# Optimization experiments

Hardware: AMD Instinct MI355X
Metric: run time of the kernel (lower is better)

## Reference

```python
import jax, jax.numpy as jnp
import numpy as np

N, E = 100000, 3200000
D_IN, D_H, H, C, TDIM, N_CLS = 17, 32, 2, 16, 32, 2


def _seg_softmax(alpha, dst, num_segments):
    # numerically stable softmax over edges grouped by destination node
    m = jax.ops.segment_max(alpha, dst, num_segments=num_segments)  # [N,H]
    a = jnp.exp(alpha - m[dst])
    s = jax.ops.segment_sum(a, dst, num_segments=num_segments)      # [N,H]
    return a / s[dst]


def setup_inputs() -> dict:
    key = jax.random.key(0)
    ks = jax.random.split(key, 16)
    w = lambda k, o, i: jax.random.normal(k, (o, i), dtype=jnp.float32) * 0.05
    inp = {
        "x": jax.random.normal(ks[0], (N, D_IN), dtype=jnp.float32),
        "edge_index": jax.random.randint(ks[1], (2, E), 0, N, dtype=jnp.int64),
        "t": jax.random.uniform(ks[2], (E, 1), dtype=jnp.float32),
        "node_time": jax.random.uniform(ks[3], (N,), dtype=jnp.float32),
        # TimeEncode params (init exactly as torch module)
        "basis_freq": jnp.asarray(1.0 / 10 ** np.linspace(0, 9, TDIM), dtype=jnp.float32),
        "phase": jnp.zeros((TDIM,), dtype=jnp.float32),
        # lin: 17 -> 32
        "W_lin": w(ks[4], D_H, D_IN), "b_lin": jnp.zeros((D_H,), jnp.float32),
        # TransformerConv(32, 16, heads=2, edge_dim=32)
        "Wq": w(ks[5], H * C, D_H), "bq": jnp.zeros((H * C,), jnp.float32),
        "Wk": w(ks[6], H * C, D_H), "bk": jnp.zeros((H * C,), jnp.float32),
        "Wv": w(ks[7], H * C, D_H), "bv": jnp.zeros((H * C,), jnp.float32),
        "We": w(ks[8], H * C, TDIM), "be": jnp.zeros((H * C,), jnp.float32),
        "Wskip": w(ks[9], H * C, D_H), "bskip": jnp.zeros((H * C,), jnp.float32),
        # out: 32 -> 2
        "W_out": w(ks[10], N_CLS, D_H), "b_out": jnp.zeros((N_CLS,), jnp.float32),
    }
    return inp


def reference(x, edge_index, t, node_time, basis_freq, phase, W_lin, b_lin,
              Wq, bq, Wk, bk, Wv, bv, We, be, Wskip, bskip, W_out, b_out):
    src, dst = edge_index[0], edge_index[1]
    n = x.shape[0]
    # relative time per edge + cosine time encoding -> [E, 32]
    rel_t = node_time[src][:, None] - t                      # [E,1]
    rel_t_enc = jnp.cos(rel_t * basis_freq[None, :] + phase[None, :])  # [E,32]
    # node MLP
    h1 = jax.nn.relu(x @ W_lin.T + b_lin)                    # [N,32]
    # TransformerConv (dropout off / eval mode)
    q = (h1 @ Wq.T + bq)[dst].reshape(-1, H, C)              # [E,H,C]
    e = (rel_t_enc @ We.T + be).reshape(-1, H, C)            # [E,H,C]
    k = (h1 @ Wk.T + bk)[src].reshape(-1, H, C) + e
    alpha = (q * k).sum(-1) / jnp.sqrt(jnp.float32(C))       # [E,H]
    alpha = _seg_softmax(alpha, dst, n)
    v = (h1 @ Wv.T + bv)[src].reshape(-1, H, C) + e          # [E,H,C]
    msg = (v * alpha[:, :, None]).reshape(-1, H * C)         # [E,32]
    agg = jax.ops.segment_sum(msg, dst, num_segments=n)      # [N,32]
    h = agg + h1 @ Wskip.T + bskip                           # root/skip connection
    logits = h @ W_out.T + b_out                             # [N,2]
    return jax.nn.log_softmax(logits, axis=1)
```

## Files before the change

kernel.cpp:

```cpp
#include <hip/hip_runtime.h>
#include <math.h>

#define D_IN 17
#define DH   32
#define TDIM 32
#define TABK 128

#define NBSH 8
#define BNODES (1 << NBSH)
#define NBKMAX 512
#define CAPB 9216
#define TILE 8192

#define SM_BYTES 53248

typedef float v2f __attribute__((ext_vector_type(2)));

__global__ __launch_bounds__(64) void build_table(
    const float* __restrict__ We, const float* __restrict__ be,
    const float* __restrict__ freq, const float* __restrict__ phase,
    float* __restrict__ table, int* __restrict__ bcur)
{
    if (blockIdx.x == 0) {
        for (int i = threadIdx.x; i < NBKMAX; i += 64) bcur[i] = 0;
    }
    int k = blockIdx.x * blockDim.x + threadIdx.x;
    if (k > TABK) return;
    float r = -1.0f + 2.0f * (float)k / (float)TABK;
    float cj[TDIM];
#pragma unroll
    for (int j = 0; j < TDIM; ++j) cj[j] = cosf(r * freq[j] + phase[j]);
#pragma unroll 4
    for (int o = 0; o < DH; ++o) {
        float acc = be[o];
#pragma unroll
        for (int j = 0; j < TDIM; ++j) acc += cj[j] * We[o * TDIM + j];
        table[(size_t)k * DH + o] = acc;
    }
}

__global__ __launch_bounds__(512) void fused_np_s1(
    const float* __restrict__ x,
    const float* __restrict__ Wl, const float* __restrict__ bl,
    const float* __restrict__ Wq, const float* __restrict__ bq,
    const float* __restrict__ Wk, const float* __restrict__ bk,
    const float* __restrict__ Wv, const float* __restrict__ bv,
    const float* __restrict__ Ws, const float* __restrict__ bs,
    float* __restrict__ qn, unsigned char* __restrict__ kvn,
    float* __restrict__ skv, int N,
    const int* __restrict__ ei, const float* __restrict__ t,
    const float* __restrict__ ntime,
    int* __restrict__ bcur, int* __restrict__ stgA,
    int E, int NBK, int NA, int NB)
{
    __shared__ __align__(16) char smraw[SM_BYTES];

    int bid = blockIdx.x;
    int tid = threadIdx.x;

    int grp = bid / 3, rem = bid - grp * 3;
    bool isA;
    int ridx;
    if (grp < NB) {
        if (rem < 2) { isA = true;  ridx = grp * 2 + rem; }
        else         { isA = false; ridx = grp; }
    } else {
        isA = true;  ridx = 2 * NB + (bid - 3 * NB);
    }

    if (isA) {
        if (ridx >= NA) return;
        float* w = (float*)smraw;
        int mat  = ridx & 3;
        int xblk = ridx >> 2;

        {
            const float* Wsel = (mat == 0) ? Wq : (mat == 1) ? Wk : (mat == 2) ? Wv : Ws;
            const float* bsel = (mat == 0) ? bq : (mat == 1) ? bk : (mat == 2) ? bv : bs;
            for (int idx = tid; idx < 544; idx += 512) {
                int i = idx / D_IN, j = idx - i * D_IN;
                w[j * DH + i] = Wl[idx];
            }
            if (tid < 32) w[544 + tid] = bl[tid];
            for (int i = tid; i < 1024; i += 512) w[576 + i] = Wsel[i];
            if (tid < 32) w[1600 + tid] = bsel[tid];
        }
        __syncthreads();

        int n = xblk * 512 + tid;
        if (n >= N) return;

        float xv[D_IN];
#pragma unroll
        for (int j = 0; j < D_IN; ++j) xv[j] = x[(size_t)n * D_IN + j];

        float h1[DH];
#pragma unroll
        for (int c = 0; c < 8; ++c) {
            float4 b = *(const float4*)&w[544 + c * 4];
            h1[c*4+0] = b.x; h1[c*4+1] = b.y; h1[c*4+2] = b.z; h1[c*4+3] = b.w;
        }
#pragma unroll
        for (int j = 0; j < D_IN; ++j) {
            float xj = xv[j];
#pragma unroll
            for (int c = 0; c < 8; ++c) {
                float4 wv = *(const float4*)&w[j * DH + c * 4];
                h1[c*4+0] += xj * wv.x;
                h1[c*4+1] += xj * wv.y;
                h1[c*4+2] += xj * wv.z;
                h1[c*4+3] += xj * wv.w;
            }
        }
#pragma unroll
        for (int i = 0; i < DH; ++i) h1[i] = fmaxf(h1[i], 0.0f);

        float outr[DH];
#pragma unroll
        for (int i = 0; i < DH; ++i) {
            float acc = w[1600 + i];
#pragma unroll
            for (int c = 0; c < 8; ++c) {
                float4 wv = *(const float4*)&w[576 + i * DH + c * 4];
                acc += h1[c * 4 + 0] * wv.x + h1[c * 4 + 1] * wv.y
                     + h1[c * 4 + 2] * wv.z + h1[c * 4 + 3] * wv.w;
            }
            outr[i] = acc;
        }

        if (mat == 0) {
            float4* dst4 = (float4*)(qn + (size_t)n * DH);
#pragma unroll
            for (int c = 0; c < 8; ++c) {
                float4 o; o.x = outr[c*4+0] * 0.25f; o.y = outr[c*4+1] * 0.25f;
                o.z = outr[c*4+2] * 0.25f; o.w = outr[c*4+3] * 0.25f;
                dst4[c] = o;
            }
        } else if (mat == 1 || mat == 2) {
            unsigned int pw[8];
#pragma unroll
            for (int i = 0; i < 8; ++i) {
                int pk = 0;
                pk = __builtin_amdgcn_cvt_pk_fp8_f32(outr[4*i+0], outr[4*i+1], pk, false);
                pk = __builtin_amdgcn_cvt_pk_fp8_f32(outr[4*i+2], outr[4*i+3], pk, true);
                pw[i] = (unsigned int)pk;
            }
            uint4* row = (uint4*)(kvn + (size_t)n * 64) + (mat == 1 ? 0 : 2);
            uint4 o0; o0.x = pw[0]; o0.y = pw[1]; o0.z = pw[2]; o0.w = pw[3];
            uint4 o1; o1.x = pw[4]; o1.y = pw[5]; o1.z = pw[6]; o1.w = pw[7];
            row[0] = o0;
            row[1] = o1;
        } else {
            float4* dst4 = (float4*)(skv + (size_t)n * DH);
#pragma unroll
            for (int c = 0; c < 8; ++c) {
                float4 o; o.x = outr[c*4+0]; o.y = outr[c*4+1];
                o.z = outr[c*4+2]; o.w = outr[c*4+3];
                dst4[c] = o;
            }
        }
        return;
    }

    int*            tileW = (int*)smraw;
    unsigned short* tileB = (unsigned short*)(smraw + 32768);
    int*            sd    = (int*)(smraw + 32768);
    int*            lcnt  = (int*)(smraw + 49152);
    int*            lcur  = (int*)(smraw + 51200);
    int*            gdel  = lcnt;

    int base = ridx * TILE;
    int cnt_here = min(TILE, E - base);

    lcnt[tid] = 0;
    __syncthreads();

    int dreg[TILE / 512];
#pragma unroll
    for (int i = 0; i < TILE / 512; ++i) {
        int e = base + i * 512 + tid;
        if (e < E) {
            int d = ei[E + e];
            dreg[i] = d;
            atomicAdd(&lcnt[((unsigned int)d) >> NBSH], 1);
        } else {
            dreg[i] = -1;
        }
    }
    __syncthreads();

    {
        int v0 = lcnt[tid];
        int lane = tid & 63, wv = tid >> 6;
        int val = v0;
#pragma unroll
        for (int st = 1; st < 64; st <<= 1) {
            int nb = __shfl_up(val, st);
            if (lane >= st) val += nb;
        }
        if (lane == 63) sd[wv] = val;
        __syncthreads();
        int woff = 0;
#pragma unroll
        for (int k2 = 0; k2 < 7; ++k2) woff += (k2 < wv) ? sd[k2] : 0;
        int lofs = woff + val - v0;
        if (tid < NBK) {
            int gpos = (v0 > 0) ? (tid * CAPB + atomicAdd(&bcur[tid], v0)) : 0;
            lcur[tid] = lofs;
            gdel[tid] = gpos - lofs;
        }
    }
    __syncthreads();

#pragma unroll 4
    for (int i = 0; i < TILE / 512; ++i) {
        int d = dreg[i];
        if (d >= 0) {
            int e = base + i * 512 + tid;
            int s = ei[e];
            float rel = ntime[s] - t[e];
            float u = fmaf(rel, (float)(TABK / 2), (float)(TABK / 2) + 0.5f);
            int idx = (int)u;
            idx = min(max(idx, 0), TABK - 1);
            int b = ((unsigned int)d) >> NBSH;
            int r = atomicAdd(&lcur[b], 1);
            tileW[r] = s | (idx << 17) | ((d & (BNODES - 1)) << 24);
            tileB[r] = (unsigned short)b;
        }
    }
    __syncthreads();

    for (int k = tid; k < cnt_here; k += 512) {
        int b = (int)tileB[k];
        int gp = gdel[b] + k;
        if (gp >= b * CAPB && gp < (b + 1) * CAPB) {
            stgA[gp] = tileW[k];
        }
    }
}

__global__ __launch_bounds__(1024) void s2_hist_scatter(
    const int* __restrict__ bcur, const int* __restrict__ stgA,
    int* __restrict__ payload, int* __restrict__ off, int* __restrict__ cntout,
    int N)
{
    __shared__ int lcnt[BNODES];
    __shared__ int sc[BNODES];
    int t = threadIdx.x;
    int nb0 = blockIdx.x << NBSH;
    if (t < BNODES) lcnt[t] = 0;
    __syncthreads();

    int lo = blockIdx.x * CAPB;
    int hi = lo + min(bcur[blockIdx.x], CAPB);

    for (int i = lo + t; i < hi; i += 1024)
        atomicAdd(&lcnt[((unsigned int)stgA[i]) >> 24], 1);
    __syncthreads();

    if (t < BNODES) sc[t] = lcnt[t];
    __syncthreads();
    for (int st = 1; st < BNODES; st <<= 1) {
        int v = 0;
        if (t < BNODES && t >= st) v = sc[t - st];
        __syncthreads();
        if (t < BNODES) sc[t] += v;
        __syncthreads();
    }
    if (t < BNODES) {
        int c = lcnt[t];
        int gpos = lo + sc[t] - c;
        if (nb0 + t < N) { off[nb0 + t] = gpos; cntout[nb0 + t] = c; }
        lcnt[t] = gpos;
    }
    __syncthreads();

    for (int i = lo + t; i < hi; i += 1024) {
        int a = stgA[i];
        int pos = atomicAdd(&lcnt[((unsigned int)a) >> 24], 1);
        payload[pos] = a;
    }
}

__global__ __launch_bounds__(256) void gather_pass(
    const int* __restrict__ off, const int* __restrict__ cnt,
    const int* __restrict__ payload,
    const float* __restrict__ qn, const unsigned char* __restrict__ kvn,
    const float* __restrict__ skv, const float* __restrict__ table,
    const float* __restrict__ Wout, const float* __restrict__ bout,
    float* __restrict__ out, int N)
{
    int tid = blockIdx.x * blockDim.x + threadIdx.x;
    int d    = tid >> 4;
    int slot = (tid >> 2) & 3;
    int sub  = tid & 3;
    if (d >= N) return;

    int qb = sub * 8;
    const float4 qa = *(const float4*)(qn + d * DH + qb);
    const float4 qc = *(const float4*)(qn + d * DH + qb + 4);

    float a0 = 0, a1 = 0, a2 = 0, a3 = 0, a4 = 0, a5 = 0, a6 = 0, a7 = 0;
    float ssum = 0.0f;

    int beg = off[d];
    int end = beg + cnt[d];
    int j = beg + slot;
    int p = (j < end) ? payload[j] : 0;
    for (; j < end; j += 4) {
        int pc = p;
        if (j + 4 < end) p = payload[j + 4];

        int src = pc & 0x1FFFF;
        int idx = (pc >> 17) & 0x7F;

        const float* tr = table + idx * DH + qb;
        float4 e0 = *(const float4*)tr;
        float4 e1 = *(const float4*)(tr + 4);
        const unsigned char* row = kvn + src * 64 + sub * 8;
        uint2 kb = *(const uint2*)row;
        uint2 vb = *(const uint2*)(row + 32);

        v2f k01 = __builtin_amdgcn_cvt_pk_f32_fp8((int)kb.x, false);
        v2f k23 = __builtin_amdgcn_cvt_pk_f32_fp8((int)kb.x, true);
        v2f k45 = __builtin_amdgcn_cvt_pk_f32_fp8((int)kb.y, false);
        v2f k67 = __builtin_amdgcn_cvt_pk_f32_fp8((int)kb.y, true);

        float part = qa.x * (k01.x + e0.x) + qa.y * (k01.y + e0.y)
                   + qa.z * (k23.x + e0.z) + qa.w * (k23.y + e0.w)
                   + qc.x * (k45.x + e1.x) + qc.y * (k45.y + e1.y)
                   + qc.z * (k67.x + e1.z) + qc.w * (k67.y + e1.w);
        part += __shfl_xor(part, 1);
        float wgt = __expf(part);
        ssum += wgt;

        v2f v01 = __builtin_amdgcn_cvt_pk_f32_fp8((int)vb.x, false);
        v2f v23 = __builtin_amdgcn_cvt_pk_f32_fp8((int)vb.x, true);
        v2f v45 = __builtin_amdgcn_cvt_pk_f32_fp8((int)vb.y, false);
        v2f v67 = __builtin_amdgcn_cvt_pk_f32_fp8((int)vb.y, true);

        a0 += (v01.x + e0.x) * wgt;
        a1 += (v01.y + e0.y) * wgt;
        a2 += (v23.x + e0.z) * wgt;
        a3 += (v23.y + e0.w) * wgt;
        a4 += (v45.x + e1.x) * wgt;
        a5 += (v45.y + e1.y) * wgt;
        a6 += (v67.x + e1.z) * wgt;
        a7 += (v67.y + e1.w) * wgt;
    }

#define COMB(dist)                                                           \
    a0 += __shfl_xor(a0, dist); a1 += __shfl_xor(a1, dist);                  \
    a2 += __shfl_xor(a2, dist); a3 += __shfl_xor(a3, dist);                  \
    a4 += __shfl_xor(a4, dist); a5 += __shfl_xor(a5, dist);                  \
    a6 += __shfl_xor(a6, dist); a7 += __shfl_xor(a7, dist);                  \
    ssum += __shfl_xor(ssum, dist);
    COMB(4)
    COMB(8)
#undef COMB

    float r = (ssum > 0.0f) ? 1.0f / ssum : 0.0f;
    const float4 ska = *(const float4*)(skv + d * DH + qb);
    const float4 skc = *(const float4*)(skv + d * DH + qb + 4);
    float h0 = a0 * r + ska.x;
    float h1 = a1 * r + ska.y;
    float h2 = a2 * r + ska.z;
    float h3 = a3 * r + ska.w;
    float h4 = a4 * r + skc.x;
    float h5 = a5 * r + skc.y;
    float h6 = a6 * r + skc.z;
    float h7 = a7 * r + skc.w;

    const float4 w0a = *(const float4*)(Wout + qb);
    const float4 w0c = *(const float4*)(Wout + qb + 4);
    const float4 w1a = *(const float4*)(Wout + DH + qb);
    const float4 w1c = *(const float4*)(Wout + DH + qb + 4);
    float l0 = h0 * w0a.x + h1 * w0a.y + h2 * w0a.z + h3 * w0a.w
             + h4 * w0c.x + h5 * w0c.y + h6 * w0c.z + h7 * w0c.w;
    float l1 = h0 * w1a.x + h1 * w1a.y + h2 * w1a.z + h3 * w1a.w
             + h4 * w1c.x + h5 * w1c.y + h6 * w1c.z + h7 * w1c.w;
    l0 += __shfl_xor(l0, 1); l0 += __shfl_xor(l0, 2);
    l1 += __shfl_xor(l1, 1); l1 += __shfl_xor(l1, 2);

    if ((tid & 15) == 0) {
        l0 += bout[0];
        l1 += bout[1];
        float m = fmaxf(l0, l1);
        float lse = m + logf(__expf(l0 - m) + __expf(l1 - m));
        float2 o; o.x = l0 - lse; o.y = l1 - lse;
        *(float2*)(out + d * 2) = o;
    }
}

extern "C" void kernel_launch(void* const* d_in, const int* in_sizes, int n_in,
                              void* d_out, int out_size, void* d_ws, size_t ws_size,
                              hipStream_t stream)
{
    const float* x      = (const float*)d_in[0];
    const int*   ei     = (const int*)d_in[1];
    const float* t      = (const float*)d_in[2];
    const float* ntime  = (const float*)d_in[3];
    const float* freq   = (const float*)d_in[4];
    const float* phase  = (const float*)d_in[5];
    const float* Wl     = (const float*)d_in[6];
    const float* bl     = (const float*)d_in[7];
    const float* Wq     = (const float*)d_in[8];
    const float* bq     = (const float*)d_in[9];
    const float* Wk     = (const float*)d_in[10];
    const float* bk     = (const float*)d_in[11];
    const float* Wv     = (const float*)d_in[12];
    const float* bv     = (const float*)d_in[13];
    const float* We     = (const float*)d_in[14];
    const float* be     = (const float*)d_in[15];
    const float* Ws     = (const float*)d_in[16];
    const float* bs     = (const float*)d_in[17];
    const float* Wout   = (const float*)d_in[18];
    const float* bout   = (const float*)d_in[19];

    const int E = in_sizes[2];
    const int N = in_sizes[3];
    const int NBK = (N + BNODES - 1) >> NBSH;

    char* wsb = (char*)d_ws;
    int*   stgA    = (int*)wsb;             wsb += (size_t)NBK * CAPB * 4;
    int*   payload = (int*)wsb;             wsb += (size_t)NBK * CAPB * 4;
    float* qn   = (float*)wsb;              wsb += (size_t)N * DH * 4;
    unsigned char* kvn = (unsigned char*)wsb; wsb += (size_t)N * 64;
    float* skv  = (float*)wsb;              wsb += (size_t)N * DH * 4;
    float* tab  = (float*)wsb;              wsb += (size_t)(TABK + 1) * DH * 4;
    int*   off  = (int*)wsb;                wsb += (size_t)N * 4;
    int*   cnt  = (int*)wsb;                wsb += (size_t)N * 4;
    int*   bcur = (int*)wsb;                wsb += NBKMAX * 4;

    float* out = (float*)d_out;

    int NA = ((N + 511) / 512) * 4;
    int NB = (E + TILE - 1) / TILE;
    int fgrid = 3 * NB + max(0, NA - 2 * NB);

    build_table<<<(TABK + 64) / 64, 64, 0, stream>>>(We, be, freq, phase, tab, bcur);
    fused_np_s1<<<fgrid, 512, 0, stream>>>(
        x, Wl, bl, Wq, bq, Wk, bk, Wv, bv, Ws, bs, qn, kvn, skv, N,
        ei, t, ntime, bcur, stgA, E, NBK, NA, NB);
    s2_hist_scatter<<<NBK, 1024, 0, stream>>>(bcur, stgA, payload, off, cnt, N);

    int gblk = ((size_t)N * 16 + 255) / 256;
    gather_pass<<<gblk, 256, 0, stream>>>(off, cnt, payload, qn, kvn, skv,
                                          tab, Wout, bout, out, N);
}
```

Baseline: 163.7 us.

## Fuse per-bucket histogram scatter with attention gather in shared memory

Merges the bucket sort (histogram, scan, scatter) and the per-node attention gather into one kernel. Each 512-thread block sorts its bucket's edge payloads into a shared-memory tile and then processes the bucket's 256 nodes, 32 at a time. This removes one kernel launch and the global payload/off/cnt round trip. In exchange the grid shrinks to one block per bucket (about 391 blocks) with 36KB+ of shared memory each, which lowers parallelism and occupancy for the gather phase.

Result: no change. 165.5 us (+1.1%).

```diff
diff --git a/kernel.cpp b/kernel.cpp
--- a/kernel.cpp
+++ b/kernel.cpp
@@ -239,156 +239,156 @@
     }
 }
 
-__global__ __launch_bounds__(1024) void s2_hist_scatter(
+__global__ __launch_bounds__(512) void s2_gather(
     const int* __restrict__ bcur, const int* __restrict__ stgA,
-    int* __restrict__ payload, int* __restrict__ off, int* __restrict__ cntout,
-    int N)
-{
-    __shared__ int lcnt[BNODES];
-    __shared__ int sc[BNODES];
-    int t = threadIdx.x;
-    int nb0 = blockIdx.x << NBSH;
-    if (t < BNODES) lcnt[t] = 0;
-    __syncthreads();
-
-    int lo = blockIdx.x * CAPB;
-    int hi = lo + min(bcur[blockIdx.x], CAPB);
-
-    for (int i = lo + t; i < hi; i += 1024)
-        atomicAdd(&lcnt[((unsigned int)stgA[i]) >> 24], 1);
-    __syncthreads();
-
-    if (t < BNODES) sc[t] = lcnt[t];
-    __syncthreads();
-    for (int st = 1; st < BNODES; st <<= 1) {
-        int v = 0;
-        if (t < BNODES && t >= st) v = sc[t - st];
-        __syncthreads();
-        if (t < BNODES) sc[t] += v;
-        __syncthreads();
-    }
-    if (t < BNODES) {
-        int c = lcnt[t];
-        int gpos = lo + sc[t] - c;
-        if (nb0 + t < N) { off[nb0 + t] = gpos; cntout[nb0 + t] = c; }
-        lcnt[t] = gpos;
-    }
-    __syncthreads();
-
-    for (int i = lo + t; i < hi; i += 1024) {
-        int a = stgA[i];
-        int pos = atomicAdd(&lcnt[((unsigned int)a) >> 24], 1);
-        payload[pos] = a;
-    }
-}
-
-__global__ __launch_bounds__(256) void gather_pass(
-    const int* __restrict__ off, const int* __restrict__ cnt,
-    const int* __restrict__ payload,
     const float* __restrict__ qn, const unsigned char* __restrict__ kvn,
     const float* __restrict__ skv, const float* __restrict__ table,
     const float* __restrict__ Wout, const float* __restrict__ bout,
     float* __restrict__ out, int N)
 {
-    int tid = blockIdx.x * blockDim.x + threadIdx.x;
-    int d    = tid >> 4;
-    int slot = (tid >> 2) & 3;
-    int sub  = tid & 3;
-    if (d >= N) return;
-
-    int qb = sub * 8;
-    const float4 qa = *(const float4*)(qn + d * DH + qb);
-    const float4 qc = *(const float4*)(qn + d * DH + qb + 4);
-
-    float a0 = 0, a1 = 0, a2 = 0, a3 = 0, a4 = 0, a5 = 0, a6 = 0, a7 = 0;
-    float ssum = 0.0f;
-
-    int beg = off[d];
-    int end = beg + cnt[d];
-    int j = beg + slot;
-    int p = (j < end) ? payload[j] : 0;
-    for (; j < end; j += 4) {
-        int pc = p;
-        if (j + 4 < end) p = payload[j + 4];
-
-        int src = pc & 0x1FFFF;
-        int idx = (pc >> 17) & 0x7F;
-
-        const float* tr = table + idx * DH + qb;
-        float4 e0 = *(const float4*)tr;
-        float4 e1 = *(const float4*)(tr + 4);
-        const unsigned char* row = kvn + src * 64 + sub * 8;
-        uint2 kb = *(const uint2*)row;
-        uint2 vb = *(const uint2*)(row + 32);
-
-        v2f k01 = __builtin_amdgcn_cvt_pk_f32_fp8((int)kb.x, false);
-        v2f k23 = __builtin_amdgcn_cvt_pk_f32_fp8((int)kb.x, true);
-        v2f k45 = __builtin_amdgcn_cvt_pk_f32_fp8((int)kb.y, false);
-        v2f k67 = __builtin_amdgcn_cvt_pk_f32_fp8((int)kb.y, true);
-
-        float part = qa.x * (k01.x + e0.x) + qa.y * (k01.y + e0.y)
-                   + qa.z * (k23.x + e0.z) + qa.w * (k23.y + e0.w)
-                   + qc.x * (k45.x + e1.x) + qc.y * (k45.y + e1.y)
-                   + qc.z * (k67.x + e1.z) + qc.w * (k67.y + e1.w);
-        part += __shfl_xor(part, 1);
-        float wgt = __expf(part);
-        ssum += wgt;
-
-        v2f v01 = __builtin_amdgcn_cvt_pk_f32_fp8((int)vb.x, false);
-        v2f v23 = __builtin_amdgcn_cvt_pk_f32_fp8((int)vb.x, true);
-        v2f v45 = __builtin_amdgcn_cvt_pk_f32_fp8((int)vb.y, false);
-        v2f v67 = __builtin_amdgcn_cvt_pk_f32_fp8((int)vb.y, true);
-
-        a0 += (v01.x + e0.x) * wgt;
-        a1 += (v01.y + e0.y) * wgt;
-        a2 += (v23.x + e0.z) * wgt;
-        a3 += (v23.y + e0.w) * wgt;
-        a4 += (v45.x + e1.x) * wgt;
-        a5 += (v45.y + e1.y) * wgt;
-        a6 += (v67.x + e1.z) * wgt;
-        a7 += (v67.y + e1.w) * wgt;
-    }
-
-#define COMB(dist)                                                           \
-    a0 += __shfl_xor(a0, dist); a1 += __shfl_xor(a1, dist);                  \
-    a2 += __shfl_xor(a2, dist); a3 += __shfl_xor(a3, dist);                  \
-    a4 += __shfl_xor(a4, dist); a5 += __shfl_xor(a5, dist);                  \
-    a6 += __shfl_xor(a6, dist); a7 += __shfl_xor(a7, dist);                  \
-    ssum += __shfl_xor(ssum, dist);
-    COMB(4)
-    COMB(8)
-#undef COMB
-
-    float r = (ssum > 0.0f) ? 1.0f / ssum : 0.0f;
-    const float4 ska = *(const float4*)(skv + d * DH + qb);
-    const float4 skc = *(const float4*)(skv + d * DH + qb + 4);
-    float h0 = a0 * r + ska.x;
-    float h1 = a1 * r + ska.y;
-    float h2 = a2 * r + ska.z;
-    float h3 = a3 * r + ska.w;
-    float h4 = a4 * r + skc.x;
-    float h5 = a5 * r + skc.y;
-    float h6 = a6 * r + skc.z;
-    float h7 = a7 * r + skc.w;
+    __shared__ int tileP[CAPB];
+    __shared__ int lcnt[BNODES];
+    __shared__ int lsta[BNODES];
+    __shared__ int lcur[BNODES];
+
+    int t = threadIdx.x;
+    int nb0 = blockIdx.x << NBSH;
+    if (t < BNODES) lcnt[t] = 0;
+    __syncthreads();
+
+    int lo = blockIdx.x * CAPB;
+    int cntb = min(bcur[blockIdx.x], CAPB);
+
+    for (int i = t; i < cntb; i += 512)
+        atomicAdd(&lcnt[((unsigned int)stgA[lo + i]) >> 24], 1);
+    __syncthreads();
+
+    if (t < BNODES) lsta[t] = lcnt[t];
+    __syncthreads();
+    for (int st = 1; st < BNODES; st <<= 1) {
+        int v = 0;
+        if (t < BNODES && t >= st) v = lsta[t - st];
+        __syncthreads();
+        if (t < BNODES) lsta[t] += v;
+        __syncthreads();
+    }
+    if (t < BNODES) {
+        int start = lsta[t] - lcnt[t];
+        lsta[t] = start;
+        lcur[t] = start;
+    }
+    __syncthreads();
+
+    for (int i = t; i < cntb; i += 512) {
+        int a = stgA[lo + i];
+        int pos = atomicAdd(&lcur[((unsigned int)a) >> 24], 1);
+        tileP[pos] = a;
+    }
+    __syncthreads();
+
+    int grp  = t >> 4;
+    int slot = (t >> 2) & 3;
+    int sub  = t & 3;
+    int qb   = sub * 8;
 
     const float4 w0a = *(const float4*)(Wout + qb);
     const float4 w0c = *(const float4*)(Wout + qb + 4);
     const float4 w1a = *(const float4*)(Wout + DH + qb);
     const float4 w1c = *(const float4*)(Wout + DH + qb + 4);
-    float l0 = h0 * w0a.x + h1 * w0a.y + h2 * w0a.z + h3 * w0a.w
-             + h4 * w0c.x + h5 * w0c.y + h6 * w0c.z + h7 * w0c.w;
-    float l1 = h0 * w1a.x + h1 * w1a.y + h2 * w1a.z + h3 * w1a.w
-             + h4 * w1c.x + h5 * w1c.y + h6 * w1c.z + h7 * w1c.w;
-    l0 += __shfl_xor(l0, 1); l0 += __shfl_xor(l0, 2);
-    l1 += __shfl_xor(l1, 1); l1 += __shfl_xor(l1, 2);
-
-    if ((tid & 15) == 0) {
-        l0 += bout[0];
-        l1 += bout[1];
-        float m = fmaxf(l0, l1);
-        float lse = m + logf(__expf(l0 - m) + __expf(l1 - m));
-        float2 o; o.x = l0 - lse; o.y = l1 - lse;
-        *(float2*)(out + d * 2) = o;
+    float bo0 = bout[0], bo1 = bout[1];
+
+#pragma unroll
+    for (int p = 0; p < BNODES / 32; ++p) {
+        int ni = p * 32 + grp;
+        int g = nb0 + ni;
+        if (g >= N) continue;
+
+        int beg = lsta[ni];
+        int end = lcur[ni];
+
+        const float4 qa = *(const float4*)(qn + (size_t)g * DH + qb);
+        const float4 qc = *(const float4*)(qn + (size_t)g * DH + qb + 4);
+
+        float a0 = 0, a1 = 0, a2 = 0, a3 = 0, a4 = 0, a5 = 0, a6 = 0, a7 = 0;
+        float ssum = 0.0f;
+
+        for (int j = beg + slot; j < end; j += 4) {
+            int pc = tileP[j];
+            int src = pc & 0x1FFFF;
+            int idx = (pc >> 17) & 0x7F;
+
+            const float* tr = table + idx * DH + qb;
+            float4 e0 = *(const float4*)tr;
+            float4 e1 = *(const float4*)(tr + 4);
+            const unsigned char* row = kvn + (size_t)src * 64 + sub * 8;
+            uint2 kb = *(const uint2*)row;
+            uint2 vb = *(const uint2*)(row + 32);
+
+            v2f k01 = __builtin_amdgcn_cvt_pk_f32_fp8((int)kb.x, false);
+            v2f k23 = __builtin_amdgcn_cvt_pk_f32_fp8((int)kb.x, true);
+            v2f k45 = __builtin_amdgcn_cvt_pk_f32_fp8((int)kb.y, false);
+            v2f k67 = __builtin_amdgcn_cvt_pk_f32_fp8((int)kb.y, true);
+
+            float part = qa.x * (k01.x + e0.x) + qa.y * (k01.y + e0.y)
+                       + qa.z * (k23.x + e0.z) + qa.w * (k23.y + e0.w)
+                       + qc.x * (k45.x + e1.x) + qc.y * (k45.y + e1.y)
+                       + qc.z * (k67.x + e1.z) + qc.w * (k67.y + e1.w);
+            part += __shfl_xor(part, 1);
+            float wgt = __expf(part);
+            ssum += wgt;
+
+            v2f v01 = __builtin_amdgcn_cvt_pk_f32_fp8((int)vb.x, false);
+            v2f v23 = __builtin_amdgcn_cvt_pk_f32_fp8((int)vb.x, true);
+            v2f v45 = __builtin_amdgcn_cvt_pk_f32_fp8((int)vb.y, false);
+            v2f v67 = __builtin_amdgcn_cvt_pk_f32_fp8((int)vb.y, true);
+
+            a0 += (v01.x + e0.x) * wgt;
+            a1 += (v01.y + e0.y) * wgt;
+            a2 += (v23.x + e0.z) * wgt;
+            a3 += (v23.y + e0.w) * wgt;
+            a4 += (v45.x + e1.x) * wgt;
+            a5 += (v45.y + e1.y) * wgt;
+            a6 += (v67.x + e1.z) * wgt;
+            a7 += (v67.y + e1.w) * wgt;
+        }
+
+#define COMB(dist)                                                           \
+        a0 += __shfl_xor(a0, dist); a1 += __shfl_xor(a1, dist);              \
+        a2 += __shfl_xor(a2, dist); a3 += __shfl_xor(a3, dist);              \
+        a4 += __shfl_xor(a4, dist); a5 += __shfl_xor(a5, dist);              \
+        a6 += __shfl_xor(a6, dist); a7 += __shfl_xor(a7, dist);              \
+        ssum += __shfl_xor(ssum, dist);
+        COMB(4)
+        COMB(8)
+#undef COMB
+
+        float r = (ssum > 0.0f) ? 1.0f / ssum : 0.0f;
+        const float4 ska = *(const float4*)(skv + (size_t)g * DH + qb);
+        const float4 skc = *(const float4*)(skv + (size_t)g * DH + qb + 4);
+        float h0 = a0 * r + ska.x;
+        float h1 = a1 * r + ska.y;
+        float h2 = a2 * r + ska.z;
+        float h3 = a3 * r + ska.w;
+        float h4 = a4 * r + skc.x;
+        float h5 = a5 * r + skc.y;
+        float h6 = a6 * r + skc.z;
+        float h7 = a7 * r + skc.w;
+
+        float l0 = h0 * w0a.x + h1 * w0a.y + h2 * w0a.z + h3 * w0a.w
+                 + h4 * w0c.x + h5 * w0c.y + h6 * w0c.z + h7 * w0c.w;
+        float l1 = h0 * w1a.x + h1 * w1a.y + h2 * w1a.z + h3 * w1a.w
+                 + h4 * w1c.x + h5 * w1c.y + h6 * w1c.z + h7 * w1c.w;
+        l0 += __shfl_xor(l0, 1); l0 += __shfl_xor(l0, 2);
+        l1 += __shfl_xor(l1, 1); l1 += __shfl_xor(l1, 2);
+
+        if ((t & 15) == 0) {
+            l0 += bo0;
+            l1 += bo1;
+            float m = fmaxf(l0, l1);
+            float lse = m + logf(__expf(l0 - m) + __expf(l1 - m));
+            float2 o; o.x = l0 - lse; o.y = l1 - lse;
+            *(float2*)(out + (size_t)g * 2) = o;
+        }
     }
 }
 
@@ -423,13 +423,10 @@
 
     char* wsb = (char*)d_ws;
     int*   stgA    = (int*)wsb;             wsb += (size_t)NBK * CAPB * 4;
-    int*   payload = (int*)wsb;             wsb += (size_t)NBK * CAPB * 4;
     float* qn   = (float*)wsb;              wsb += (size_t)N * DH * 4;
     unsigned char* kvn = (unsigned char*)wsb; wsb += (size_t)N * 64;
     float* skv  = (float*)wsb;              wsb += (size_t)N * DH * 4;
     float* tab  = (float*)wsb;              wsb += (size_t)(TABK + 1) * DH * 4;
-    int*   off  = (int*)wsb;                wsb += (size_t)N * 4;
-    int*   cnt  = (int*)wsb;                wsb += (size_t)N * 4;
     int*   bcur = (int*)wsb;                wsb += NBKMAX * 4;
 
     float* out = (float*)d_out;
@@ -442,9 +439,6 @@
     fused_np_s1<<<fgrid, 512, 0, stream>>>(
         x, Wl, bl, Wq, bq, Wk, bk, Wv, bv, Ws, bs, qn, kvn, skv, N,
         ei, t, ntime, bcur, stgA, E, NBK, NA, NB);
-    s2_hist_scatter<<<NBK, 1024, 0, stream>>>(bcur, stgA, payload, off, cnt, N);
-
-    int gblk = ((size_t)N * 16 + 255) / 256;
-    gather_pass<<<gblk, 256, 0, stream>>>(off, cnt, payload, qn, kvn, skv,
-                                          tab, Wout, bout, out, N);
+    s2_gather<<<NBK, 512, 0, stream>>>(bcur, stgA, qn, kvn, skv, tab,
+                                       Wout, bout, out, N);
 }
```
